# Performance work log

Hardware: AMD Instinct MI355X
Metric: run time of the kernel (lower is better)

The kernel has to match this reference:

```python
import jax, jax.numpy as jnp
import numpy as np

PAST = 12
FUTURE = 12


def setup_inputs() -> dict:
    key = jax.random.key(0)
    k1, k2, k3, k4, k5 = jax.random.split(key, 5)
    B, L, D = 64, 256, 512
    inp = jax.random.normal(k1, (B, L, D), dtype=jnp.float32)
    W_t = jax.random.normal(k2, (FUTURE, PAST), dtype=jnp.float32) / np.sqrt(PAST)
    b_t = jax.random.normal(k3, (FUTURE,), dtype=jnp.float32) * 0.01
    W_s = jax.random.normal(k4, (D, D), dtype=jnp.float32) / np.sqrt(D)
    b_s = jax.random.normal(k5, (D,), dtype=jnp.float32) * 0.01
    return {"inp": inp, "W_t": W_t, "b_t": b_t, "W_s": W_s, "b_s": b_s}


def reference(inp, W_t, b_t, W_s, b_s):
    # inp: [B, L, D]. Sliding windows of size PAST -> W = L - PAST windows.
    B, L, D = inp.shape
    W = L - PAST
    # gather windows: [B, W, PAST, D]
    idx = jnp.arange(W)[:, None] + jnp.arange(PAST)[None, :]  # [W, PAST]
    x_win = inp[:, idx, :]  # [B, W, PAST, D]
    # temporal Linear(PAST -> FUTURE) along window-time axis
    t = jnp.einsum('bwpd,fp->bwfd', x_win, W_t) + b_t[None, None, :, None]
    # spatial Linear(D -> D) along last axis
    out = jnp.einsum('bwfd,ed->bwfe', t, W_s) + b_s
    return out  # [B, W, FUTURE, D]
```

## Files before the change

kernel.cpp:

```cpp
#include <hip/hip_runtime.h>

#define PAST 12
#define FUTURE 12
#define NB 64
#define NL 256
#define ND 512
#define NW 244

typedef unsigned short ushort_t;
typedef __attribute__((ext_vector_type(8))) short short8;
typedef __attribute__((ext_vector_type(4))) float floatx4;

__device__ inline unsigned int f2bf(float x) {
    unsigned int u = __float_as_uint(x);
    return (u + 0x7fffu + ((u >> 16) & 1u)) >> 16;
}

__global__ __launch_bounds__(256) void convert_inp(
    const float* __restrict__ in, ushort_t* __restrict__ out)
{
    const int swz = (blockIdx.x & 7) * 512 + (blockIdx.x >> 3);
    const int i = (swz * 256 + threadIdx.x) * 8;
    const float4 v0 = *(const float4*)(in + i);
    const float4 v1 = *(const float4*)(in + i + 4);
    uint4 o;
    o.x = f2bf(v0.x) | (f2bf(v0.y) << 16);
    o.y = f2bf(v0.z) | (f2bf(v0.w) << 16);
    o.z = f2bf(v1.x) | (f2bf(v1.y) << 16);
    o.w = f2bf(v1.z) | (f2bf(v1.w) << 16);
    *(uint4*)(out + i) = o;
}

__global__ __launch_bounds__(256) void prep_ws(
    const float* __restrict__ Ws, ushort_t* __restrict__ Wsb, float* __restrict__ S)
{
    const int row = blockIdx.x;
    const int t = threadIdx.x;
    const float2 v = *(const float2*)(Ws + (size_t)row * ND + t * 2);
    *(unsigned int*)(Wsb + (size_t)row * ND + t * 2) = f2bf(v.x) | (f2bf(v.y) << 16);
    float s = v.x + v.y;
#pragma unroll
    for (int o = 32; o > 0; o >>= 1) s += __shfl_down(s, o);
    __shared__ float red[4];
    if ((t & 63) == 0) red[t >> 6] = s;
    __syncthreads();
    if (t == 0) S[row] = red[0] + red[1] + red[2] + red[3];
}

#define BM 64
#define BN 64

__global__ __launch_bounds__(256) void gemm_spatial(
    const ushort_t* __restrict__ A,
    const ushort_t* __restrict__ Bm,
    ushort_t* __restrict__ Y)
{
    const int tid  = threadIdx.x;
    const int wave = tid >> 6;
    const int lane = tid & 63;

    const int bid = blockIdx.x;
    const int idx = (bid & 7) * 256 + (bid >> 3);
    const int n0 = (idx & 7) * BN;
    const int m0 = (idx >> 3) * BM;
    const int wm = (wave >> 1) * 32;
    const int wn = (wave & 1) * 32;

    const ushort_t* a0 = A  + (size_t)(m0 + wm + (lane & 15)) * ND + (lane >> 4) * 8;
    const ushort_t* b0 = Bm + (size_t)(n0 + wn + (lane & 15)) * ND + (lane >> 4) * 8;

    floatx4 acc[2][2] = {};

#pragma unroll 4
    for (int k0 = 0; k0 < ND; k0 += 32) {
        short8 af[2], bq[2];
        af[0] = *(const short8*)(a0 + k0);
        af[1] = *(const short8*)(a0 + (size_t)16 * ND + k0);
        bq[0] = *(const short8*)(b0 + k0);
        bq[1] = *(const short8*)(b0 + (size_t)16 * ND + k0);
#pragma unroll
        for (int i = 0; i < 2; ++i)
#pragma unroll
            for (int j = 0; j < 2; ++j)
                acc[i][j] = __builtin_amdgcn_mfma_f32_16x16x32_bf16(af[i], bq[j], acc[i][j], 0, 0, 0);
    }

#pragma unroll
    for (int i = 0; i < 2; ++i) {
        const int m_base = m0 + wm + i * 16 + (lane >> 4) * 4;
#pragma unroll
        for (int j = 0; j < 2; ++j) {
            const int n = n0 + wn + j * 16 + (lane & 15);
#pragma unroll
            for (int r = 0; r < 4; ++r) {
                Y[(size_t)(m_base + r) * ND + n] = (ushort_t)f2bf(acc[i][j][r]);
            }
        }
    }
}

#define WTILE 8
#define TGRID (((NW + WTILE - 1) / WTILE) * NB)

__global__ __launch_bounds__(256) void temporal_kernel(
    const ushort_t* __restrict__ Y,
    const float*    __restrict__ Wt,
    const float*    __restrict__ bt,
    const float*    __restrict__ bs,
    const float*    __restrict__ S,
    float*          __restrict__ Out)
{
    const int tid = threadIdx.x;
    const int bid = blockIdx.x;
    const int idx = (bid & 7) * (TGRID / 8) + (bid >> 3);
    const int b   = idx / 31;
    const int wx  = idx % 31;
    const int w0 = wx * WTILE + (tid >> 7) * 4;
    const int eq = (tid & 127) * 4;

    const float4 Sv  = *(const float4*)(S + eq);
    const float4 bsv = *(const float4*)(bs + eq);

    float win[PAST + 3][4];
    const ushort_t* ybase = Y + ((size_t)(b * NL + w0)) * ND + eq;
#pragma unroll
    for (int i = 0; i < PAST + 3; ++i) {
        if (w0 + i < NL) {
            const uint2 v = *(const uint2*)(ybase + (size_t)i * ND);
            win[i][0] = __uint_as_float(v.x << 16);
            win[i][1] = __uint_as_float(v.x & 0xffff0000u);
            win[i][2] = __uint_as_float(v.y << 16);
            win[i][3] = __uint_as_float(v.y & 0xffff0000u);
        } else {
            win[i][0] = win[i][1] = win[i][2] = win[i][3] = 0.f;
        }
    }

#pragma unroll
    for (int w = 0; w < 4; ++w) {
        if (w0 + w < NW) {
            float* orow = Out + ((size_t)(b * NW + (w0 + w)) * FUTURE) * ND + eq;
#pragma unroll
            for (int f = 0; f < FUTURE; ++f) {
                const float btf = bt[f];
                float a0 = fmaf(btf, Sv.x, bsv.x);
                float a1 = fmaf(btf, Sv.y, bsv.y);
                float a2 = fmaf(btf, Sv.z, bsv.z);
                float a3 = fmaf(btf, Sv.w, bsv.w);
#pragma unroll
                for (int p = 0; p < PAST; ++p) {
                    const float c = Wt[f * PAST + p];
                    a0 = fmaf(c, win[w + p][0], a0);
                    a1 = fmaf(c, win[w + p][1], a1);
                    a2 = fmaf(c, win[w + p][2], a2);
                    a3 = fmaf(c, win[w + p][3], a3);
                }
                floatx4 ov;
                ov.x = a0; ov.y = a1; ov.z = a2; ov.w = a3;
                __builtin_nontemporal_store(ov, (floatx4*)(orow + (size_t)f * ND));
            }
        }
    }
}

extern "C" void kernel_launch(void* const* d_in, const int* in_sizes, int n_in,
                              void* d_out, int out_size, void* d_ws, size_t ws_size,
                              hipStream_t stream) {
    const float* inp = (const float*)d_in[0];
    const float* Wt  = (const float*)d_in[1];
    const float* bt  = (const float*)d_in[2];
    const float* Ws  = (const float*)d_in[3];
    const float* bs  = (const float*)d_in[4];
    float* out = (float*)d_out;

    const size_t n_inp = (size_t)NB * NL * ND;
    ushort_t* Y     = (ushort_t*)d_ws;
    ushort_t* inp_b = (ushort_t*)((char*)d_ws + n_inp * 2);
    ushort_t* Ws_b  = (ushort_t*)((char*)d_ws + n_inp * 4);
    float*    S     = (float*)((char*)d_ws + n_inp * 4 + (size_t)ND * ND * 2);

    prep_ws<<<dim3(ND), dim3(256), 0, stream>>>(Ws, Ws_b, S);
    convert_inp<<<dim3(n_inp / 8 / 256), dim3(256), 0, stream>>>(inp, inp_b);
    gemm_spatial<<<dim3((NB * NL / BM) * (ND / BN)), dim3(256), 0, stream>>>(inp_b, Ws_b, Y);
    temporal_kernel<<<dim3(TGRID), dim3(256), 0, stream>>>(Y, Wt, bt, bs, S, out);
}
```

Before: 475.8 us.

## Stage spatial GEMM through triple-buffered LDS with async global-to-LDS loads

The spatial GEMM now uses 128x64 tiles and stages A and B K-slices into three LDS buffers with global_load_lds. Each step issues the tile two iterations ahead before computing the current one, using explicit waitcnt and barrier instructions. Before, every wave loaded its MFMA operands straight from global memory without reuse. This is meant to hide load latency and share fragments across waves, at the cost of more LDS, fewer blocks, and fragile hand-written wait counts.

```diff
diff --git a/kernel.cpp b/kernel.cpp
--- a/kernel.cpp
+++ b/kernel.cpp
@@ -47,46 +47,94 @@
     if (t == 0) S[row] = red[0] + red[1] + red[2] + red[3];
 }
 
-#define BM 64
+#define BM 128
 #define BN 64
+#define BK 32
 
 __global__ __launch_bounds__(256) void gemm_spatial(
     const ushort_t* __restrict__ A,
     const ushort_t* __restrict__ Bm,
     ushort_t* __restrict__ Y)
 {
+    __shared__ __align__(16) ushort_t lds[3 * (BM * BK + BN * BK)];
+
     const int tid  = threadIdx.x;
     const int wave = tid >> 6;
     const int lane = tid & 63;
 
     const int bid = blockIdx.x;
-    const int idx = (bid & 7) * 256 + (bid >> 3);
+    const int idx = (bid & 7) * 128 + (bid >> 3);
     const int n0 = (idx & 7) * BN;
     const int m0 = (idx >> 3) * BM;
-    const int wm = (wave >> 1) * 32;
+    const int wm = (wave >> 1) * 64;
     const int wn = (wave & 1) * 32;
 
-    const ushort_t* a0 = A  + (size_t)(m0 + wm + (lane & 15)) * ND + (lane >> 4) * 8;
-    const ushort_t* b0 = Bm + (size_t)(n0 + wn + (lane & 15)) * ND + (lane >> 4) * 8;
-
-    floatx4 acc[2][2] = {};
-
-#pragma unroll 4
-    for (int k0 = 0; k0 < ND; k0 += 32) {
-        short8 af[2], bq[2];
-        af[0] = *(const short8*)(a0 + k0);
-        af[1] = *(const short8*)(a0 + (size_t)16 * ND + k0);
-        bq[0] = *(const short8*)(b0 + k0);
-        bq[1] = *(const short8*)(b0 + (size_t)16 * ND + k0);
-#pragma unroll
-        for (int i = 0; i < 2; ++i)
-#pragma unroll
-            for (int j = 0; j < 2; ++j)
-                acc[i][j] = __builtin_amdgcn_mfma_f32_16x16x32_bf16(af[i], bq[j], acc[i][j], 0, 0, 0);
-    }
-
-#pragma unroll
-    for (int i = 0; i < 2; ++i) {
+    ushort_t* const As0 = lds;
+    ushort_t* const Bs0 = lds + BM * BK;
+    ushort_t* const As1 = lds + 6144;
+    ushort_t* const Bs1 = lds + 6144 + BM * BK;
+    ushort_t* const As2 = lds + 12288;
+    ushort_t* const Bs2 = lds + 12288 + BM * BK;
+
+    const ushort_t* ga0 = A  + (size_t)(m0 + (tid >> 2)) * ND + (tid & 3) * 8;
+    const ushort_t* ga1 = ga0 + (size_t)64 * ND;
+    const ushort_t* gb0 = Bm + (size_t)(n0 + (tid >> 2)) * ND + (tid & 3) * 8;
+
+#define ISSUE_TILE(Asb, Bsb, k0) do { \
+    __builtin_amdgcn_global_load_lds( \
+        (const __attribute__((address_space(1))) unsigned int*)(ga0 + (k0)), \
+        (__attribute__((address_space(3))) unsigned int*)((Asb) + tid * 8), 16, 0, 0); \
+    __builtin_amdgcn_global_load_lds( \
+        (const __attribute__((address_space(1))) unsigned int*)(ga1 + (k0)), \
+        (__attribute__((address_space(3))) unsigned int*)((Asb) + 2048 + tid * 8), 16, 0, 0); \
+    __builtin_amdgcn_global_load_lds( \
+        (const __attribute__((address_space(1))) unsigned int*)(gb0 + (k0)), \
+        (__attribute__((address_space(3))) unsigned int*)((Bsb) + tid * 8), 16, 0, 0); \
+} while (0)
+
+#define COMPUTE_TILE(Asb, Bsb) do { \
+    const ushort_t* a_base = (Asb) + (wm + (lane & 15)) * BK + (lane >> 4) * 8; \
+    const ushort_t* b_base = (Bsb) + (wn + (lane & 15)) * BK + (lane >> 4) * 8; \
+    short8 af[4], bq[2]; \
+    _Pragma("unroll") \
+    for (int t = 0; t < 4; ++t) af[t] = *(const short8*)(a_base + t * 16 * BK); \
+    _Pragma("unroll") \
+    for (int t = 0; t < 2; ++t) bq[t] = *(const short8*)(b_base + t * 16 * BK); \
+    _Pragma("unroll") \
+    for (int i = 0; i < 4; ++i) \
+    _Pragma("unroll") \
+    for (int j = 0; j < 2; ++j) \
+        acc[i][j] = __builtin_amdgcn_mfma_f32_16x16x32_bf16(af[i], bq[j], acc[i][j], 0, 0, 0); \
+} while (0)
+
+#define STEP(c, n, k) do { \
+    asm volatile("s_waitcnt vmcnt(3) lgkmcnt(0)\n\ts_barrier" ::: "memory"); \
+    __builtin_amdgcn_sched_barrier(0); \
+    if ((k) + 2 < 16) ISSUE_TILE(As##n, Bs##n, ((k) + 2) * BK); \
+    COMPUTE_TILE(As##c, Bs##c); \
+} while (0)
+
+    floatx4 acc[4][2] = {};
+
+    ISSUE_TILE(As0, Bs0, 0);
+    ISSUE_TILE(As1, Bs1, BK);
+
+    for (int t = 0; t < 5; ++t) {
+        const int k = t * 3;
+        STEP(0, 2, k);
+        STEP(1, 0, k + 1);
+        STEP(2, 1, k + 2);
+    }
+    asm volatile("s_waitcnt vmcnt(0) lgkmcnt(0)\n\ts_barrier" ::: "memory");
+    __builtin_amdgcn_sched_barrier(0);
+    COMPUTE_TILE(As0, Bs0);
+
+#undef STEP
+#undef ISSUE_TILE
+#undef COMPUTE_TILE
+
+#pragma unroll
+    for (int i = 0; i < 4; ++i) {
         const int m_base = m0 + wm + i * 16 + (lane >> 4) * 4;
 #pragma unroll
         for (int j = 0; j < 2; ++j) {
```

New measurement: 431.7 us. 1.1x faster.
